# Kernel tuning notes

Hardware: AMD Instinct MI355X
Metric: run time of the kernel (lower is better)

Reference implementation:

```python
import jax, jax.numpy as jnp
import numpy as np

N_TOKENS = 16384
HIDDEN = 1024
FFN = 4096
N_EXPERTS = 8
TOP_K = 2


def setup_inputs() -> dict:
    key = jax.random.key(0)
    k_x, k_r, k_w1, k_w2 = jax.random.split(key, 4)
    x = jax.random.normal(k_x, (N_TOKENS, HIDDEN), dtype=jnp.float32)
    w_router = jax.random.normal(k_r, (HIDDEN, N_EXPERTS), dtype=jnp.float32) * (HIDDEN ** -0.5)
    w1 = jax.random.normal(k_w1, (N_EXPERTS, HIDDEN, FFN), dtype=jnp.float32) * (HIDDEN ** -0.5)
    w2 = jax.random.normal(k_w2, (N_EXPERTS, FFN, HIDDEN), dtype=jnp.float32) * (FFN ** -0.5)
    return {"x": x, "w_router": w_router, "w1": w1, "w2": w2}


def reference(x, w_router, w1, w2):
    # --- TopKRouter: softmax over experts, take top-k, renormalize ---
    logits = x @ w_router                              # [N, E]
    probs = jax.nn.softmax(logits, axis=-1)
    topk_w, topk_idx = jax.lax.top_k(probs, TOP_K)     # [N, K]
    topk_w = topk_w / jnp.sum(topk_w, axis=-1, keepdims=True)

    # --- dispatch -> per-expert FFN -> weighted combine ---
    # Single-device equivalent: the all-to-all + sort/unsort (pt_dispatch/
    # pt_combine) form an identity permutation pair, so the math reduces to:
    # out[n] = sum_k topk_w[n,k] * FFN_{topk_idx[n,k]}(x[n])
    out = jnp.zeros_like(x)
    n_experts = w1.shape[0]
    for e in range(n_experts):  # small fixed expert loop (grouped GEMM)
        # combine weight this expert contributes to each token
        coeff = jnp.sum(jnp.where(topk_idx == e, topk_w, 0.0), axis=-1)  # [N]
        y = jax.nn.gelu(x @ w1[e]) @ w2[e]                               # [N, H]
        out = out + coeff[:, None] * y
    return out
```

## Files before the change

kernel.cpp:

```cpp
#include <hip/hip_runtime.h>
#include <cstdint>
#include <cstddef>

#define N_TOKENS 16384
#define HIDDEN 1024
#define FFN 4096
#define NEXP 8
#define BM 128
#define BK 32
#define MAXR (N_TOKENS*2 + NEXP*BM)
#define MAXTILES (MAXR/BM)

typedef __bf16 bf16;
typedef __attribute__((ext_vector_type(8))) __bf16 bf16x8;
typedef __attribute__((ext_vector_type(4))) __bf16 bf16x4;
typedef __attribute__((ext_vector_type(4))) float f32x4;

__device__ __forceinline__ void gload16(const void* g, void* l) {
  __builtin_amdgcn_global_load_lds((const __attribute__((address_space(1))) void*)g,
                                   (__attribute__((address_space(3))) void*)l, 16, 0, 0);
}

__device__ __forceinline__ int xcd_swz(int orig, int nwg) {
  int q = nwg >> 3, r = nwg & 7;
  int xcd = orig & 7, idx = orig >> 3;
  int base = (xcd < r) ? xcd * (q + 1) : r * (q + 1) + (xcd - r) * q;
  return base + idx;
}


__global__ __launch_bounds__(256) void convx_k(const float* __restrict__ x,
                                               bf16* __restrict__ xb) {
  int i = blockIdx.x * 256 + threadIdx.x;
  float4 v = reinterpret_cast<const float4*>(x)[i];
  bf16x4 o = { (bf16)v.x, (bf16)v.y, (bf16)v.z, (bf16)v.w };
  *reinterpret_cast<bf16x4*>(xb + (size_t)i * 4) = o;
}

__global__ __launch_bounds__(256) void transconv_k(const float* __restrict__ src,
                                                   bf16* __restrict__ dst,
                                                   int R, int C) {
  __shared__ float tile[64][65];
  int bx = blockIdx.x * 64;
  int by = blockIdx.y * 64;
  const float* s = src + (size_t)blockIdx.z * R * C;
  bf16* d = dst + (size_t)blockIdx.z * R * C;
  int tid = threadIdx.x;
  int tc = (tid & 15) * 4;
  int tr = tid >> 4;
  #pragma unroll
  for (int p = 0; p < 4; ++p) {
    int r = p * 16 + tr;
    float4 v = *reinterpret_cast<const float4*>(s + (size_t)(by + r) * C + bx + tc);
    tile[r][tc] = v.x; tile[r][tc + 1] = v.y; tile[r][tc + 2] = v.z; tile[r][tc + 3] = v.w;
  }
  __syncthreads();
  int wr = (tid & 15) * 4;
  int wc = tid >> 4;
  #pragma unroll
  for (int p = 0; p < 4; ++p) {
    int c = p * 16 + wc;
    bf16x4 o = { (bf16)tile[wr][c], (bf16)tile[wr + 1][c],
                 (bf16)tile[wr + 2][c], (bf16)tile[wr + 3][c] };
    *reinterpret_cast<bf16x4*>(d + (size_t)(bx + c) * R + by + wr) = o;
  }
}


__global__ __launch_bounds__(256) void logits_k(const float* __restrict__ x,
                                                const float* __restrict__ wrt,
                                                double* __restrict__ logitsE) {
  __shared__ float wT[NEXP][HIDDEN + 1];
  int tid = threadIdx.x;
  for (int i = tid; i < HIDDEN * NEXP; i += 256) {
    int k = i >> 3, e = i & 7;
    wT[e][k] = wrt[i];
  }
  __syncthreads();
  int t = blockIdx.x * 32 + (tid >> 3);
  int e = tid & 7;
  int goff = ((tid >> 3) & 7) * 4;
  const float* xr = x + (size_t)t * HIDDEN;
  double acc = 0.0;
  #pragma unroll 4
  for (int k = 0; k < HIDDEN; k += 4) {
    int kk = (k + goff) & (HIDDEN - 1);
    float4 v = *reinterpret_cast<const float4*>(xr + kk);
    acc += (double)v.x * (double)wT[e][kk];
    acc += (double)v.y * (double)wT[e][kk + 1];
    acc += (double)v.z * (double)wT[e][kk + 2];
    acc += (double)v.w * (double)wT[e][kk + 3];
  }
  logitsE[(size_t)e * N_TOKENS + t] = acc;
}


__global__ __launch_bounds__(256) void route_k(const double* __restrict__ logitsE,
                                               int* __restrict__ expIdx,
                                               float* __restrict__ expW,
                                               int* __restrict__ counts) {
  __shared__ int lcnt[NEXP];
  int tid = threadIdx.x;
  if (tid < NEXP) lcnt[tid] = 0;
  __syncthreads();
  int n = blockIdx.x * 256 + tid;
  double lg[NEXP];
  #pragma unroll
  for (int e = 0; e < NEXP; ++e) lg[e] = logitsE[(size_t)e * N_TOKENS + n];
  int e1 = 0;
  #pragma unroll
  for (int e = 1; e < NEXP; ++e) if (lg[e] > lg[e1]) e1 = e;
  int e2 = (e1 == 0) ? 1 : 0;
  #pragma unroll
  for (int e = 0; e < NEXP; ++e)
    if (e != e1 && e != e2 && lg[e] > lg[e2]) e2 = e;
  double d = lg[e2] - lg[e1];
  float w1v = (float)(1.0 / (1.0 + exp(d)));
  expIdx[2 * n]     = e1; expIdx[2 * n + 1] = e2;
  expW[2 * n]       = w1v; expW[2 * n + 1]  = 1.0f - w1v;
  atomicAdd(&lcnt[e1], 1);
  atomicAdd(&lcnt[e2], 1);
  __syncthreads();
  if (tid < NEXP) atomicAdd(&counts[tid], lcnt[tid]);
}


__global__ void offsets_k(const int* __restrict__ counts,
                          int* __restrict__ padOff, int* __restrict__ cursor) {
  if (threadIdx.x == 0) {
    int o = 0;
    for (int e = 0; e < NEXP; ++e) {
      padOff[e] = o;
      o += ((counts[e] + BM - 1) / BM) * BM;
    }
    padOff[NEXP] = o;
  }
  if (threadIdx.x < NEXP) cursor[threadIdx.x] = 0;
}

__global__ __launch_bounds__(256) void scatter_k(const int* __restrict__ expIdx,
                                                 const float* __restrict__ expW,
                                                 const int* __restrict__ padOff,
                                                 int* __restrict__ cursor,
                                                 int* __restrict__ rowTok,
                                                 float* __restrict__ rowW,
                                                 int* __restrict__ tokRow) {
  __shared__ int lcnt[NEXP], lbase[NEXP];
  int tid = threadIdx.x;
  if (tid < NEXP) lcnt[tid] = 0;
  __syncthreads();
  int n = blockIdx.x * 256 + tid;
  int e0 = expIdx[2 * n], e1 = expIdx[2 * n + 1];
  float w0 = expW[2 * n], w1 = expW[2 * n + 1];
  int p0 = atomicAdd(&lcnt[e0], 1);
  int p1 = atomicAdd(&lcnt[e1], 1);
  __syncthreads();
  if (tid < NEXP) lbase[tid] = atomicAdd(&cursor[tid], lcnt[tid]);
  __syncthreads();
  int r0 = padOff[e0] + lbase[e0] + p0;
  int r1 = padOff[e1] + lbase[e1] + p1;
  rowTok[r0] = n;  rowW[r0] = w0;  tokRow[2 * n]     = r0;
  rowTok[r1] = n;  rowW[r1] = w1;  tokRow[2 * n + 1] = r1;
}


__device__ __forceinline__ float gelu_tanh(float v) {
  float c = 0.7978845608028654f * (v + 0.044715f * v * v * v);
  c = fminf(fmaxf(c, -15.f), 15.f);
  float ex = __expf(2.f * c);
  float t = (ex - 1.f) / (ex + 1.f);
  return 0.5f * v * (1.f + t);
}

__global__ __launch_bounds__(256, 2) void gemm1_k(const bf16* __restrict__ xb,
                                                  const bf16* __restrict__ w1bT,
                                                  bf16* __restrict__ h,
                                                  const int* __restrict__ rowTok,
                                                  const int* __restrict__ padOff,
                                                  int tileStart, int rowStart) {
  __shared__ __attribute__((aligned(16))) bf16 As[BM * BK];
  __shared__ __attribute__((aligned(16))) bf16 Bs[BM * BK];
  const int nCT = FFN / 128;
  int wg = xcd_swz((int)blockIdx.x, (int)gridDim.x);
  int bt = tileStart + wg / nCT;
  int ct = wg % nCT;
  int r0 = bt * BM;
  if (r0 >= padOff[NEXP]) return;
  int e = 0;
  while (padOff[e + 1] <= r0) ++e;

  int tid = threadIdx.x;
  int lane = tid & 63, wave = tid >> 6;
  const bf16* Bbase = w1bT + ((size_t)e * FFN + (size_t)ct * 128) * HIDDEN;

  const bf16* aSrc[2]; const bf16* bSrc[2]; int ldsOff[2];
  #pragma unroll
  for (int j = 0; j < 2; ++j) {
    int ci = wave * 128 + j * 64 + lane;
    int r = ci >> 2, s = ci & 3;
    int ks = s ^ ((r >> 1) & 3);
    int tok = rowTok[r0 + r]; if (tok < 0) tok = 0;
    aSrc[j] = xb + (size_t)tok * HIDDEN + ks * 8;
    bSrc[j] = Bbase + (size_t)r * HIDDEN + ks * 8;
    ldsOff[j] = (wave * 128 + j * 64) * 8;
  }
  int g = lane >> 4, lr = lane & 15;
  int wr = wave >> 1, wc = wave & 1;
  int aOff[4], bOff[4];
  #pragma unroll
  for (int m = 0; m < 4; ++m) { int r = wr * 64 + m * 16 + lr; aOff[m] = r * BK + ((g ^ ((r >> 1) & 3)) << 3); }
  #pragma unroll
  for (int n = 0; n < 4; ++n) { int r = wc * 64 + n * 16 + lr; bOff[n] = r * BK + ((g ^ ((r >> 1) & 3)) << 3); }

  f32x4 zero = {0.f, 0.f, 0.f, 0.f};
  f32x4 acc[4][4];
  #pragma unroll
  for (int m = 0; m < 4; ++m)
    #pragma unroll
    for (int n = 0; n < 4; ++n) acc[m][n] = zero;

  for (int k0 = 0; k0 < HIDDEN; k0 += BK) {
    #pragma unroll
    for (int j = 0; j < 2; ++j) {
      gload16(aSrc[j] + k0, &As[ldsOff[j]]);
      gload16(bSrc[j] + k0, &Bs[ldsOff[j]]);
    }
    __syncthreads();
    bf16x8 af[4], bfr[4];
    #pragma unroll
    for (int m = 0; m < 4; ++m) af[m] = *reinterpret_cast<const bf16x8*>(&As[aOff[m]]);
    #pragma unroll
    for (int n = 0; n < 4; ++n) bfr[n] = *reinterpret_cast<const bf16x8*>(&Bs[bOff[n]]);
    #pragma unroll
    for (int m = 0; m < 4; ++m)
      #pragma unroll
      for (int n = 0; n < 4; ++n)
        acc[m][n] = __builtin_amdgcn_mfma_f32_16x16x32_bf16(af[m], bfr[n], acc[m][n], 0, 0, 0);
    __syncthreads();
  }

  int colBase = ct * 128 + wc * 64 + lr;
  #pragma unroll
  for (int m = 0; m < 4; ++m) {
    #pragma unroll
    for (int i = 0; i < 4; ++i) {
      int t = r0 + wr * 64 + m * 16 + g * 4 + i;
      bf16* hp = h + (size_t)(t - rowStart) * FFN + colBase;
      #pragma unroll
      for (int n = 0; n < 4; ++n)
        hp[n * 16] = (bf16)gelu_tanh(acc[m][n][i]);
    }
  }
}


__global__ __launch_bounds__(256, 2) void gemm2_k(const bf16* __restrict__ h,
                                                  const bf16* __restrict__ w2bT,
                                                  float* __restrict__ y,
                                                  const int* __restrict__ padOff,
                                                  int tileStart, int rowStart) {
  __shared__ __attribute__((aligned(16))) bf16 As[BM * BK];
  __shared__ __attribute__((aligned(16))) bf16 Bs[BM * BK];
  const int nCT = HIDDEN / 128;
  int wg = xcd_swz((int)blockIdx.x, (int)gridDim.x);
  int bt = tileStart + wg / nCT;
  int ct = wg % nCT;
  int r0 = bt * BM;
  if (r0 >= padOff[NEXP]) return;
  int e = 0;
  while (padOff[e + 1] <= r0) ++e;

  int tid = threadIdx.x;
  int lane = tid & 63, wave = tid >> 6;
  const bf16* Bbase = w2bT + ((size_t)e * HIDDEN + (size_t)ct * 128) * FFN;
  const bf16* Arow = h + (size_t)(r0 - rowStart) * FFN;

  const bf16* aSrc[2]; const bf16* bSrc[2]; int ldsOff[2];
  #pragma unroll
  for (int j = 0; j < 2; ++j) {
    int ci = wave * 128 + j * 64 + lane;
    int r = ci >> 2, s = ci & 3;
    int ks = s ^ ((r >> 1) & 3);
    aSrc[j] = Arow + (size_t)r * FFN + ks * 8;
    bSrc[j] = Bbase + (size_t)r * FFN + ks * 8;
    ldsOff[j] = (wave * 128 + j * 64) * 8;
  }
  int g = lane >> 4, lr = lane & 15;
  int wr = wave >> 1, wc = wave & 1;
  int aOff[4], bOff[4];
  #pragma unroll
  for (int m = 0; m < 4; ++m) { int r = wr * 64 + m * 16 + lr; aOff[m] = r * BK + ((g ^ ((r >> 1) & 3)) << 3); }
  #pragma unroll
  for (int n = 0; n < 4; ++n) { int r = wc * 64 + n * 16 + lr; bOff[n] = r * BK + ((g ^ ((r >> 1) & 3)) << 3); }

  f32x4 zero = {0.f, 0.f, 0.f, 0.f};
  f32x4 acc[4][4];
  #pragma unroll
  for (int m = 0; m < 4; ++m)
    #pragma unroll
    for (int n = 0; n < 4; ++n) acc[m][n] = zero;

  for (int k0 = 0; k0 < FFN; k0 += BK) {
    #pragma unroll
    for (int j = 0; j < 2; ++j) {
      gload16(aSrc[j] + k0, &As[ldsOff[j]]);
      gload16(bSrc[j] + k0, &Bs[ldsOff[j]]);
    }
    __syncthreads();
    bf16x8 af[4], bfr[4];
    #pragma unroll
    for (int m = 0; m < 4; ++m) af[m] = *reinterpret_cast<const bf16x8*>(&As[aOff[m]]);
    #pragma unroll
    for (int n = 0; n < 4; ++n) bfr[n] = *reinterpret_cast<const bf16x8*>(&Bs[bOff[n]]);
    #pragma unroll
    for (int m = 0; m < 4; ++m)
      #pragma unroll
      for (int n = 0; n < 4; ++n)
        acc[m][n] = __builtin_amdgcn_mfma_f32_16x16x32_bf16(af[m], bfr[n], acc[m][n], 0, 0, 0);
    __syncthreads();
  }

  int colBase = ct * 128 + wc * 64 + lr;
  #pragma unroll
  for (int m = 0; m < 4; ++m) {
    #pragma unroll
    for (int i = 0; i < 4; ++i) {
      int t = r0 + wr * 64 + m * 16 + g * 4 + i;
      float* yp = y + (size_t)t * HIDDEN + colBase;
      #pragma unroll
      for (int n = 0; n < 4; ++n)
        yp[n * 16] = acc[m][n][i];
    }
  }
}


__global__ __launch_bounds__(256) void combine_k(const float* __restrict__ y,
                                                 const int* __restrict__ tokRow,
                                                 const float* __restrict__ rowW,
                                                 float* __restrict__ out) {
  int n = blockIdx.x;
  int c = threadIdx.x * 4;
  int r0 = tokRow[2 * n], r1 = tokRow[2 * n + 1];
  float w0 = rowW[r0], w1 = rowW[r1];
  float4 a = *reinterpret_cast<const float4*>(y + (size_t)r0 * HIDDEN + c);
  float4 b = *reinterpret_cast<const float4*>(y + (size_t)r1 * HIDDEN + c);
  float4 o = { w0 * a.x + w1 * b.x, w0 * a.y + w1 * b.y,
               w0 * a.z + w1 * b.z, w0 * a.w + w1 * b.w };
  *reinterpret_cast<float4*>(out + (size_t)n * HIDDEN + c) = o;
}


extern "C" void kernel_launch(void* const* d_in, const int* in_sizes, int n_in,
                              void* d_out, int out_size, void* d_ws, size_t ws_size,
                              hipStream_t stream) {
  const float* x   = (const float*)d_in[0];
  const float* wrt = (const float*)d_in[1];
  const float* w1  = (const float*)d_in[2];
  const float* w2  = (const float*)d_in[3];
  float* out = (float*)d_out;

  char* p = (char*)d_ws;
  size_t off = 0;
  auto alloc = [&](size_t bytes) -> void* {
    void* r = p + off;
    off = (off + bytes + 255) & ~(size_t)255;
    return r;
  };

  int*    counts  = (int*)   alloc(NEXP * 4);
  int*    padOff  = (int*)   alloc((NEXP + 1) * 4);
  int*    cursor  = (int*)   alloc(NEXP * 4);
  int*    expIdx  = (int*)   alloc((size_t)N_TOKENS * 2 * 4);
  float*  expW    = (float*) alloc((size_t)N_TOKENS * 2 * 4);
  int*    rowTok  = (int*)   alloc((size_t)MAXR * 4);
  float*  rowW    = (float*) alloc((size_t)MAXR * 4);
  int*    tokRow  = (int*)   alloc((size_t)N_TOKENS * 2 * 4);
  double* logitsE = (double*)alloc((size_t)NEXP * N_TOKENS * 8);
  bf16*   xb      = (bf16*)  alloc((size_t)N_TOKENS * HIDDEN * 2);
  bf16*   w1bT    = (bf16*)  alloc((size_t)NEXP * FFN * HIDDEN * 2);
  bf16*   w2bT    = (bf16*)  alloc((size_t)NEXP * FFN * HIDDEN * 2);
  float*  y       = (float*) alloc((size_t)MAXR * HIDDEN * 4);
  size_t fixed = off;
  bf16* h = (bf16*)(p + fixed);

  size_t tileB = (size_t)BM * FFN * 2;
  size_t avail = (ws_size > fixed) ? (ws_size - fixed) : tileB;
  size_t fitSz = avail / tileB;
  int tilesFit = (int)((fitSz < (size_t)MAXTILES) ? fitSz : (size_t)MAXTILES);
  if (tilesFit < 1) tilesFit = 1;
  int nchunks = (MAXTILES + tilesFit - 1) / tilesFit;
  int tpc = (MAXTILES + nchunks - 1) / nchunks;

  hipMemsetAsync(counts, 0, NEXP * 4, stream);
  hipMemsetAsync(rowTok, 0xFF, (size_t)MAXR * 4, stream);

  convx_k<<<N_TOKENS * HIDDEN / 4 / 256, 256, 0, stream>>>(x, xb);
  transconv_k<<<dim3(FFN / 64, HIDDEN / 64, NEXP), dim3(256, 1, 1), 0, stream>>>(w1, w1bT, HIDDEN, FFN);
  transconv_k<<<dim3(HIDDEN / 64, FFN / 64, NEXP), dim3(256, 1, 1), 0, stream>>>(w2, w2bT, FFN, HIDDEN);
  logits_k<<<N_TOKENS / 32, 256, 0, stream>>>(x, wrt, logitsE);
  route_k<<<N_TOKENS / 256, 256, 0, stream>>>(logitsE, expIdx, expW, counts);
  offsets_k<<<1, 64, 0, stream>>>(counts, padOff, cursor);
  scatter_k<<<N_TOKENS / 256, 256, 0, stream>>>(expIdx, expW, padOff, cursor, rowTok, rowW, tokRow);

  for (int c = 0; c < nchunks; ++c) {
    int ts = c * tpc;
    int rs = ts * BM;
    gemm1_k<<<tpc * (FFN / 128), 256, 0, stream>>>(xb, w1bT, h, rowTok, padOff, ts, rs);
    gemm2_k<<<tpc * (HIDDEN / 128), 256, 0, stream>>>(h, w2bT, y, padOff, ts, rs);
  }
  combine_k<<<N_TOKENS, 256, 0, stream>>>(y, tokRow, rowW, out);
}
```

Measured before the change: 1.015 ms.

## Use 256x256 tiles with a 4-stage async LDS pipeline and bf16 expert outputs

```diff
diff --git a/kernel.cpp b/kernel.cpp
--- a/kernel.cpp
+++ b/kernel.cpp
@@ -6,10 +6,10 @@
 #define HIDDEN 1024
 #define FFN 4096
 #define NEXP 8
-#define BM 128
+#define BM2 256
 #define BK 32
-#define MAXR (N_TOKENS*2 + NEXP*BM)
-#define MAXTILES (MAXR/BM)
+#define MAXR (N_TOKENS*2 + NEXP*BM2)
+#define MAXTILES (MAXR/BM2)
 
 typedef __bf16 bf16;
 typedef __attribute__((ext_vector_type(8))) __bf16 bf16x8;
@@ -131,7 +131,7 @@
     int o = 0;
     for (int e = 0; e < NEXP; ++e) {
       padOff[e] = o;
-      o += ((counts[e] + BM - 1) / BM) * BM;
+      o += ((counts[e] + BM2 - 1) / BM2) * BM2;
     }
     padOff[NEXP] = o;
   }
@@ -164,6 +164,74 @@
 }
 
 
+#define GEMM_PROLOGUE(AROWPTR_EXPR, BROW_STRIDE)                               \
+  int tid = threadIdx.x;                                                       \
+  int lane = tid & 63, wave = tid >> 6;                                        \
+  int wm = wave >> 2, wn = wave & 3;                                           \
+  int lr = lane & 15, g = lane >> 4;                                           \
+  const bf16* aPtr[2]; const bf16* bPtr[2];                                    \
+  int aLds[2], bLds[2];                                                        \
+  _Pragma("unroll")                                                            \
+  for (int j = 0; j < 2; ++j) {                                                \
+    int ci = j * 512 + tid;                                                    \
+    int r = ci >> 2, s = ci & 3;                                               \
+    int ks = s ^ (r & 3);                                                      \
+    aPtr[j] = (AROWPTR_EXPR) + ks * 8;                                         \
+    bPtr[j] = Bbase + (size_t)r * (BROW_STRIDE) + ks * 8;                      \
+    aLds[j] = j * 4096 + wave * 512;                                           \
+    bLds[j] = j * 4096 + wave * 512;                                           \
+  }                                                                            \
+  int aRd = (wm * 128 + lr) * BK + ((g ^ (lr & 3)) << 3);                      \
+  int bRd = (wn * 64 + lr) * BK + ((g ^ (lr & 3)) << 3);                       \
+  f32x4 acc[8][4];                                                             \
+  _Pragma("unroll")                                                            \
+  for (int m = 0; m < 8; ++m)                                                  \
+    _Pragma("unroll")                                                          \
+    for (int n = 0; n < 4; ++n) acc[m][n] = (f32x4){0.f, 0.f, 0.f, 0.f};
+
+#define STAGE(kt, b) do {                                                      \
+    gload16(aPtr[0] + (size_t)(kt) * BK, &Ab[b][aLds[0]]);                     \
+    gload16(aPtr[1] + (size_t)(kt) * BK, &Ab[b][aLds[1]]);                     \
+    gload16(bPtr[0] + (size_t)(kt) * BK, &Bb[b][bLds[0]]);                     \
+    gload16(bPtr[1] + (size_t)(kt) * BK, &Bb[b][bLds[1]]);                     \
+  } while (0)
+
+#define GEMM_KLOOP(NT)                                                         \
+  STAGE(0, 0); STAGE(1, 1); STAGE(2, 2);                                       \
+  _Pragma("unroll 1")                                                          \
+  for (int kt = 0; kt < (NT); ++kt) {                                          \
+    int b = kt & 3;                                                            \
+    int pf = kt + 3;                                                           \
+    if (pf < (NT)) STAGE(pf, pf & 3);                                          \
+    int rem = (NT) - 1 - kt;                                                   \
+    if (rem >= 3)      asm volatile("s_waitcnt vmcnt(12)" ::: "memory");       \
+    else if (rem == 2) asm volatile("s_waitcnt vmcnt(8)" ::: "memory");        \
+    else if (rem == 1) asm volatile("s_waitcnt vmcnt(4)" ::: "memory");        \
+    else               asm volatile("s_waitcnt vmcnt(0)" ::: "memory");        \
+    __builtin_amdgcn_sched_barrier(0);                                         \
+    __builtin_amdgcn_s_barrier();                                              \
+    __builtin_amdgcn_sched_barrier(0);                                         \
+    bf16x8 af[8], bf[4];                                                       \
+    _Pragma("unroll")                                                          \
+    for (int m = 0; m < 8; ++m)                                                \
+      af[m] = *reinterpret_cast<const bf16x8*>(&Ab[b][aRd + m * 512]);         \
+    _Pragma("unroll")                                                          \
+    for (int n = 0; n < 4; ++n)                                                \
+      bf[n] = *reinterpret_cast<const bf16x8*>(&Bb[b][bRd + n * 512]);         \
+    __builtin_amdgcn_s_setprio(1);                                             \
+    _Pragma("unroll")                                                          \
+    for (int m = 0; m < 8; ++m)                                                \
+      _Pragma("unroll")                                                        \
+      for (int n = 0; n < 4; ++n)                                              \
+        acc[m][n] = __builtin_amdgcn_mfma_f32_16x16x32_bf16(af[m], bf[n],      \
+                                                            acc[m][n], 0, 0, 0); \
+    __builtin_amdgcn_s_setprio(0);                                             \
+    __builtin_amdgcn_sched_barrier(0);                                         \
+    __builtin_amdgcn_s_barrier();                                              \
+    __builtin_amdgcn_sched_barrier(0);                                         \
+  }
+
+
 __device__ __forceinline__ float gelu_tanh(float v) {
   float c = 0.7978845608028654f * (v + 0.044715f * v * v * v);
   c = fminf(fmaxf(c, -15.f), 15.f);
@@ -172,79 +240,34 @@
   return 0.5f * v * (1.f + t);
 }
 
-__global__ __launch_bounds__(256, 2) void gemm1_k(const bf16* __restrict__ xb,
+__global__ __launch_bounds__(512, 2) void gemm1_k(const bf16* __restrict__ xb,
                                                   const bf16* __restrict__ w1bT,
                                                   bf16* __restrict__ h,
                                                   const int* __restrict__ rowTok,
                                                   const int* __restrict__ padOff,
                                                   int tileStart, int rowStart) {
-  __shared__ __attribute__((aligned(16))) bf16 As[BM * BK];
-  __shared__ __attribute__((aligned(16))) bf16 Bs[BM * BK];
-  const int nCT = FFN / 128;
+  __shared__ __attribute__((aligned(16))) bf16 Ab[4][256 * BK];
+  __shared__ __attribute__((aligned(16))) bf16 Bb[4][256 * BK];
+  const int nCT = FFN / 256;
   int wg = xcd_swz((int)blockIdx.x, (int)gridDim.x);
   int bt = tileStart + wg / nCT;
   int ct = wg % nCT;
-  int r0 = bt * BM;
+  int r0 = bt * BM2;
   if (r0 >= padOff[NEXP]) return;
   int e = 0;
   while (padOff[e + 1] <= r0) ++e;
-
-  int tid = threadIdx.x;
-  int lane = tid & 63, wave = tid >> 6;
-  const bf16* Bbase = w1bT + ((size_t)e * FFN + (size_t)ct * 128) * HIDDEN;
-
-  const bf16* aSrc[2]; const bf16* bSrc[2]; int ldsOff[2];
-  #pragma unroll
-  for (int j = 0; j < 2; ++j) {
-    int ci = wave * 128 + j * 64 + lane;
-    int r = ci >> 2, s = ci & 3;
-    int ks = s ^ ((r >> 1) & 3);
-    int tok = rowTok[r0 + r]; if (tok < 0) tok = 0;
-    aSrc[j] = xb + (size_t)tok * HIDDEN + ks * 8;
-    bSrc[j] = Bbase + (size_t)r * HIDDEN + ks * 8;
-    ldsOff[j] = (wave * 128 + j * 64) * 8;
-  }
-  int g = lane >> 4, lr = lane & 15;
-  int wr = wave >> 1, wc = wave & 1;
-  int aOff[4], bOff[4];
-  #pragma unroll
-  for (int m = 0; m < 4; ++m) { int r = wr * 64 + m * 16 + lr; aOff[m] = r * BK + ((g ^ ((r >> 1) & 3)) << 3); }
-  #pragma unroll
-  for (int n = 0; n < 4; ++n) { int r = wc * 64 + n * 16 + lr; bOff[n] = r * BK + ((g ^ ((r >> 1) & 3)) << 3); }
-
-  f32x4 zero = {0.f, 0.f, 0.f, 0.f};
-  f32x4 acc[4][4];
-  #pragma unroll
-  for (int m = 0; m < 4; ++m)
-    #pragma unroll
-    for (int n = 0; n < 4; ++n) acc[m][n] = zero;
-
-  for (int k0 = 0; k0 < HIDDEN; k0 += BK) {
-    #pragma unroll
-    for (int j = 0; j < 2; ++j) {
-      gload16(aSrc[j] + k0, &As[ldsOff[j]]);
-      gload16(bSrc[j] + k0, &Bs[ldsOff[j]]);
-    }
-    __syncthreads();
-    bf16x8 af[4], bfr[4];
-    #pragma unroll
-    for (int m = 0; m < 4; ++m) af[m] = *reinterpret_cast<const bf16x8*>(&As[aOff[m]]);
-    #pragma unroll
-    for (int n = 0; n < 4; ++n) bfr[n] = *reinterpret_cast<const bf16x8*>(&Bs[bOff[n]]);
-    #pragma unroll
-    for (int m = 0; m < 4; ++m)
-      #pragma unroll
-      for (int n = 0; n < 4; ++n)
-        acc[m][n] = __builtin_amdgcn_mfma_f32_16x16x32_bf16(af[m], bfr[n], acc[m][n], 0, 0, 0);
-    __syncthreads();
-  }
-
-  int colBase = ct * 128 + wc * 64 + lr;
-  #pragma unroll
-  for (int m = 0; m < 4; ++m) {
+  const bf16* Bbase = w1bT + ((size_t)e * FFN + (size_t)ct * 256) * HIDDEN;
+
+  GEMM_PROLOGUE(xb + (size_t)(rowTok[r0 + r] < 0 ? 0 : rowTok[r0 + r]) * HIDDEN,
+                HIDDEN)
+  GEMM_KLOOP(HIDDEN / BK)
+
+  int colBase = ct * 256 + wn * 64 + lr;
+  #pragma unroll
+  for (int m = 0; m < 8; ++m) {
     #pragma unroll
     for (int i = 0; i < 4; ++i) {
-      int t = r0 + wr * 64 + m * 16 + g * 4 + i;
+      int t = r0 + wm * 128 + m * 16 + g * 4 + i;
       bf16* hp = h + (size_t)(t - rowStart) * FFN + colBase;
       #pragma unroll
       for (int n = 0; n < 4; ++n)
@@ -254,88 +277,42 @@
 }
 
 
-__global__ __launch_bounds__(256, 2) void gemm2_k(const bf16* __restrict__ h,
+__global__ __launch_bounds__(512, 2) void gemm2_k(const bf16* __restrict__ h,
                                                   const bf16* __restrict__ w2bT,
-                                                  float* __restrict__ y,
+                                                  bf16* __restrict__ y,
                                                   const int* __restrict__ padOff,
                                                   int tileStart, int rowStart) {
-  __shared__ __attribute__((aligned(16))) bf16 As[BM * BK];
-  __shared__ __attribute__((aligned(16))) bf16 Bs[BM * BK];
-  const int nCT = HIDDEN / 128;
+  __shared__ __attribute__((aligned(16))) bf16 Ab[4][256 * BK];
+  __shared__ __attribute__((aligned(16))) bf16 Bb[4][256 * BK];
+  const int nCT = HIDDEN / 256;
   int wg = xcd_swz((int)blockIdx.x, (int)gridDim.x);
   int bt = tileStart + wg / nCT;
   int ct = wg % nCT;
-  int r0 = bt * BM;
+  int r0 = bt * BM2;
   if (r0 >= padOff[NEXP]) return;
   int e = 0;
   while (padOff[e + 1] <= r0) ++e;
-
-  int tid = threadIdx.x;
-  int lane = tid & 63, wave = tid >> 6;
-  const bf16* Bbase = w2bT + ((size_t)e * HIDDEN + (size_t)ct * 128) * FFN;
-  const bf16* Arow = h + (size_t)(r0 - rowStart) * FFN;
-
-  const bf16* aSrc[2]; const bf16* bSrc[2]; int ldsOff[2];
-  #pragma unroll
-  for (int j = 0; j < 2; ++j) {
-    int ci = wave * 128 + j * 64 + lane;
-    int r = ci >> 2, s = ci & 3;
-    int ks = s ^ ((r >> 1) & 3);
-    aSrc[j] = Arow + (size_t)r * FFN + ks * 8;
-    bSrc[j] = Bbase + (size_t)r * FFN + ks * 8;
-    ldsOff[j] = (wave * 128 + j * 64) * 8;
-  }
-  int g = lane >> 4, lr = lane & 15;
-  int wr = wave >> 1, wc = wave & 1;
-  int aOff[4], bOff[4];
-  #pragma unroll
-  for (int m = 0; m < 4; ++m) { int r = wr * 64 + m * 16 + lr; aOff[m] = r * BK + ((g ^ ((r >> 1) & 3)) << 3); }
-  #pragma unroll
-  for (int n = 0; n < 4; ++n) { int r = wc * 64 + n * 16 + lr; bOff[n] = r * BK + ((g ^ ((r >> 1) & 3)) << 3); }
-
-  f32x4 zero = {0.f, 0.f, 0.f, 0.f};
-  f32x4 acc[4][4];
-  #pragma unroll
-  for (int m = 0; m < 4; ++m)
+  const bf16* Bbase = w2bT + ((size_t)e * HIDDEN + (size_t)ct * 256) * FFN;
+
+  GEMM_PROLOGUE(h + (size_t)(r0 - rowStart + r) * FFN, FFN)
+  GEMM_KLOOP(FFN / BK)
+
+  int colBase = ct * 256 + wn * 64 + lr;
+  #pragma unroll
+  for (int m = 0; m < 8; ++m) {
     #pragma unroll
-    for (int n = 0; n < 4; ++n) acc[m][n] = zero;
-
-  for (int k0 = 0; k0 < FFN; k0 += BK) {
-    #pragma unroll
-    for (int j = 0; j < 2; ++j) {
-      gload16(aSrc[j] + k0, &As[ldsOff[j]]);
-      gload16(bSrc[j] + k0, &Bs[ldsOff[j]]);
-    }
-    __syncthreads();
-    bf16x8 af[4], bfr[4];
-    #pragma unroll
-    for (int m = 0; m < 4; ++m) af[m] = *reinterpret_cast<const bf16x8*>(&As[aOff[m]]);
-    #pragma unroll
-    for (int n = 0; n < 4; ++n) bfr[n] = *reinterpret_cast<const bf16x8*>(&Bs[bOff[n]]);
-    #pragma unroll
-    for (int m = 0; m < 4; ++m)
+    for (int i = 0; i < 4; ++i) {
+      int t = r0 + wm * 128 + m * 16 + g * 4 + i;
+      bf16* yp = y + (size_t)t * HIDDEN + colBase;
       #pragma unroll
       for (int n = 0; n < 4; ++n)
-        acc[m][n] = __builtin_amdgcn_mfma_f32_16x16x32_bf16(af[m], bfr[n], acc[m][n], 0, 0, 0);
-    __syncthreads();
-  }
-
-  int colBase = ct * 128 + wc * 64 + lr;
-  #pragma unroll
-  for (int m = 0; m < 4; ++m) {
-    #pragma unroll
-    for (int i = 0; i < 4; ++i) {
-      int t = r0 + wr * 64 + m * 16 + g * 4 + i;
-      float* yp = y + (size_t)t * HIDDEN + colBase;
-      #pragma unroll
-      for (int n = 0; n < 4; ++n)
-        yp[n * 16] = acc[m][n][i];
+        yp[n * 16] = (bf16)acc[m][n][i];
     }
   }
 }
 
 
-__global__ __launch_bounds__(256) void combine_k(const float* __restrict__ y,
+__global__ __launch_bounds__(256) void combine_k(const bf16* __restrict__ y,
                                                  const int* __restrict__ tokRow,
                                                  const float* __restrict__ rowW,
                                                  float* __restrict__ out) {
@@ -343,10 +320,10 @@
   int c = threadIdx.x * 4;
   int r0 = tokRow[2 * n], r1 = tokRow[2 * n + 1];
   float w0 = rowW[r0], w1 = rowW[r1];
-  float4 a = *reinterpret_cast<const float4*>(y + (size_t)r0 * HIDDEN + c);
-  float4 b = *reinterpret_cast<const float4*>(y + (size_t)r1 * HIDDEN + c);
-  float4 o = { w0 * a.x + w1 * b.x, w0 * a.y + w1 * b.y,
-               w0 * a.z + w1 * b.z, w0 * a.w + w1 * b.w };
+  bf16x4 a = *reinterpret_cast<const bf16x4*>(y + (size_t)r0 * HIDDEN + c);
+  bf16x4 b = *reinterpret_cast<const bf16x4*>(y + (size_t)r1 * HIDDEN + c);
+  float4 o = { w0 * (float)a[0] + w1 * (float)b[0], w0 * (float)a[1] + w1 * (float)b[1],
+               w0 * (float)a[2] + w1 * (float)b[2], w0 * (float)a[3] + w1 * (float)b[3] };
   *reinterpret_cast<float4*>(out + (size_t)n * HIDDEN + c) = o;
 }
 
@@ -380,11 +357,11 @@
   bf16*   xb      = (bf16*)  alloc((size_t)N_TOKENS * HIDDEN * 2);
   bf16*   w1bT    = (bf16*)  alloc((size_t)NEXP * FFN * HIDDEN * 2);
   bf16*   w2bT    = (bf16*)  alloc((size_t)NEXP * FFN * HIDDEN * 2);
-  float*  y       = (float*) alloc((size_t)MAXR * HIDDEN * 4);
+  bf16*   y       = (bf16*)  alloc((size_t)MAXR * HIDDEN * 2);
   size_t fixed = off;
   bf16* h = (bf16*)(p + fixed);
 
-  size_t tileB = (size_t)BM * FFN * 2;
+  size_t tileB = (size_t)BM2 * FFN * 2;
   size_t avail = (ws_size > fixed) ? (ws_size - fixed) : tileB;
   size_t fitSz = avail / tileB;
   int tilesFit = (int)((fitSz < (size_t)MAXTILES) ? fitSz : (size_t)MAXTILES);
@@ -405,9 +382,9 @@
 
   for (int c = 0; c < nchunks; ++c) {
     int ts = c * tpc;
-    int rs = ts * BM;
-    gemm1_k<<<tpc * (FFN / 128), 256, 0, stream>>>(xb, w1bT, h, rowTok, padOff, ts, rs);
-    gemm2_k<<<tpc * (HIDDEN / 128), 256, 0, stream>>>(h, w2bT, y, padOff, ts, rs);
+    int rs = ts * BM2;
+    gemm1_k<<<tpc * (FFN / 256), 512, 0, stream>>>(xb, w1bT, h, rowTok, padOff, ts, rs);
+    gemm2_k<<<tpc * (HIDDEN / 256), 512, 0, stream>>>(h, w2bT, y, padOff, ts, rs);
   }
   combine_k<<<N_TOKENS, 256, 0, stream>>>(y, tokRow, rowW, out);
 }
```

Measured after the change: 1.206 ms. +18.8%, slower.

## Triple-buffer LDS loads in expert GEMMs and store expert outputs as bf16

Applied to the files above, without the earlier changes.

```diff
diff --git a/kernel.cpp b/kernel.cpp
--- a/kernel.cpp
+++ b/kernel.cpp
@@ -7,7 +7,7 @@
 #define FFN 4096
 #define NEXP 8
 #define BM 128
-#define BK 32
+#define BKS 32
 #define MAXR (N_TOKENS*2 + NEXP*BM)
 #define MAXTILES (MAXR/BM)
 
@@ -172,14 +172,14 @@
   return 0.5f * v * (1.f + t);
 }
 
-__global__ __launch_bounds__(256, 2) void gemm1_k(const bf16* __restrict__ xb,
+__global__ __launch_bounds__(256, 3) void gemm1_k(const bf16* __restrict__ xb,
                                                   const bf16* __restrict__ w1bT,
                                                   bf16* __restrict__ h,
                                                   const int* __restrict__ rowTok,
                                                   const int* __restrict__ padOff,
                                                   int tileStart, int rowStart) {
-  __shared__ __attribute__((aligned(16))) bf16 As[BM * BK];
-  __shared__ __attribute__((aligned(16))) bf16 Bs[BM * BK];
+  __shared__ __attribute__((aligned(16))) bf16 Ab[3][BM * BKS];
+  __shared__ __attribute__((aligned(16))) bf16 Bb[3][BM * BKS];
   const int nCT = FFN / 128;
   int wg = xcd_swz((int)blockIdx.x, (int)gridDim.x);
   int bt = tileStart + wg / nCT;
@@ -188,63 +188,78 @@
   if (r0 >= padOff[NEXP]) return;
   int e = 0;
   while (padOff[e + 1] <= r0) ++e;
+  const bf16* Bbase = w1bT + ((size_t)e * FFN + (size_t)ct * 128) * HIDDEN;
 
   int tid = threadIdx.x;
   int lane = tid & 63, wave = tid >> 6;
-  const bf16* Bbase = w1bT + ((size_t)e * FFN + (size_t)ct * 128) * HIDDEN;
-
-  const bf16* aSrc[2]; const bf16* bSrc[2]; int ldsOff[2];
+  const bf16* aPtr[2]; const bf16* bPtr[2]; int ldsOff[2];
   #pragma unroll
   for (int j = 0; j < 2; ++j) {
-    int ci = wave * 128 + j * 64 + lane;
-    int r = ci >> 2, s = ci & 3;
-    int ks = s ^ ((r >> 1) & 3);
+    int ci = j * 256 + tid;
+    int r = ci >> 2, sg = ci & 3;
+    int ks = sg ^ ((r >> 1) & 3);
     int tok = rowTok[r0 + r]; if (tok < 0) tok = 0;
-    aSrc[j] = xb + (size_t)tok * HIDDEN + ks * 8;
-    bSrc[j] = Bbase + (size_t)r * HIDDEN + ks * 8;
-    ldsOff[j] = (wave * 128 + j * 64) * 8;
-  }
-  int g = lane >> 4, lr = lane & 15;
-  int wr = wave >> 1, wc = wave & 1;
+    aPtr[j] = xb + (size_t)tok * HIDDEN + ks * 8;
+    bPtr[j] = Bbase + (size_t)r * HIDDEN + ks * 8;
+    ldsOff[j] = ci * 8;
+  }
+  int lr = lane & 15, g = lane >> 4;
+  int wm = wave >> 1, wn = wave & 1;
   int aOff[4], bOff[4];
   #pragma unroll
-  for (int m = 0; m < 4; ++m) { int r = wr * 64 + m * 16 + lr; aOff[m] = r * BK + ((g ^ ((r >> 1) & 3)) << 3); }
-  #pragma unroll
-  for (int n = 0; n < 4; ++n) { int r = wc * 64 + n * 16 + lr; bOff[n] = r * BK + ((g ^ ((r >> 1) & 3)) << 3); }
-
-  f32x4 zero = {0.f, 0.f, 0.f, 0.f};
+  for (int m = 0; m < 4; ++m) { int r = wm * 64 + m * 16 + lr; aOff[m] = r * BKS + ((g ^ ((r >> 1) & 3)) << 3); }
+  #pragma unroll
+  for (int n = 0; n < 4; ++n) { int r = wn * 64 + n * 16 + lr; bOff[n] = r * BKS + ((g ^ ((r >> 1) & 3)) << 3); }
+
   f32x4 acc[4][4];
   #pragma unroll
   for (int m = 0; m < 4; ++m)
     #pragma unroll
-    for (int n = 0; n < 4; ++n) acc[m][n] = zero;
-
-  for (int k0 = 0; k0 < HIDDEN; k0 += BK) {
-    #pragma unroll
-    for (int j = 0; j < 2; ++j) {
-      gload16(aSrc[j] + k0, &As[ldsOff[j]]);
-      gload16(bSrc[j] + k0, &Bs[ldsOff[j]]);
-    }
-    __syncthreads();
+    for (int n = 0; n < 4; ++n) acc[m][n] = (f32x4){0.f, 0.f, 0.f, 0.f};
+
+  const int NT = HIDDEN / BKS;
+  auto stage = [&](int sl, int b) {
+    #pragma unroll
+    for (int j = 0; j < 2; ++j) gload16(aPtr[j] + (size_t)sl * BKS, &Ab[b][ldsOff[j]]);
+    #pragma unroll
+    for (int j = 0; j < 2; ++j) gload16(bPtr[j] + (size_t)sl * BKS, &Bb[b][ldsOff[j]]);
+  };
+  stage(0, 0); stage(1, 1);
+  int buf = 0, sbuf = 2;
+  #pragma unroll 1
+  for (int s = 0; s < NT; ++s) {
+    if (s + 2 < NT) stage(s + 2, sbuf);
+    if (s < NT - 2)       asm volatile("s_waitcnt vmcnt(8)" ::: "memory");
+    else if (s == NT - 2) asm volatile("s_waitcnt vmcnt(4)" ::: "memory");
+    else                  asm volatile("s_waitcnt vmcnt(0)" ::: "memory");
+    __builtin_amdgcn_sched_barrier(0);
+    __builtin_amdgcn_s_barrier();
+    __builtin_amdgcn_sched_barrier(0);
     bf16x8 af[4], bfr[4];
     #pragma unroll
-    for (int m = 0; m < 4; ++m) af[m] = *reinterpret_cast<const bf16x8*>(&As[aOff[m]]);
-    #pragma unroll
-    for (int n = 0; n < 4; ++n) bfr[n] = *reinterpret_cast<const bf16x8*>(&Bs[bOff[n]]);
+    for (int m = 0; m < 4; ++m) af[m] = *reinterpret_cast<const bf16x8*>(&Ab[buf][aOff[m]]);
+    #pragma unroll
+    for (int n = 0; n < 4; ++n) bfr[n] = *reinterpret_cast<const bf16x8*>(&Bb[buf][bOff[n]]);
+    __builtin_amdgcn_s_setprio(1);
     #pragma unroll
     for (int m = 0; m < 4; ++m)
       #pragma unroll
       for (int n = 0; n < 4; ++n)
         acc[m][n] = __builtin_amdgcn_mfma_f32_16x16x32_bf16(af[m], bfr[n], acc[m][n], 0, 0, 0);
-    __syncthreads();
-  }
-
-  int colBase = ct * 128 + wc * 64 + lr;
+    __builtin_amdgcn_s_setprio(0);
+    __builtin_amdgcn_sched_barrier(0);
+    __builtin_amdgcn_s_barrier();
+    __builtin_amdgcn_sched_barrier(0);
+    buf = (buf == 2) ? 0 : buf + 1;
+    sbuf = (sbuf == 2) ? 0 : sbuf + 1;
+  }
+
+  int colBase = ct * 128 + wn * 64 + lr;
   #pragma unroll
   for (int m = 0; m < 4; ++m) {
     #pragma unroll
     for (int i = 0; i < 4; ++i) {
-      int t = r0 + wr * 64 + m * 16 + g * 4 + i;
+      int t = r0 + wm * 64 + m * 16 + g * 4 + i;
       bf16* hp = h + (size_t)(t - rowStart) * FFN + colBase;
       #pragma unroll
       for (int n = 0; n < 4; ++n)
@@ -253,14 +268,13 @@
   }
 }
 
-
-__global__ __launch_bounds__(256, 2) void gemm2_k(const bf16* __restrict__ h,
+__global__ __launch_bounds__(256, 3) void gemm2_k(const bf16* __restrict__ h,
                                                   const bf16* __restrict__ w2bT,
-                                                  float* __restrict__ y,
+                                                  bf16* __restrict__ y,
                                                   const int* __restrict__ padOff,
                                                   int tileStart, int rowStart) {
-  __shared__ __attribute__((aligned(16))) bf16 As[BM * BK];
-  __shared__ __attribute__((aligned(16))) bf16 Bs[BM * BK];
+  __shared__ __attribute__((aligned(16))) bf16 Ab[3][BM * BKS];
+  __shared__ __attribute__((aligned(16))) bf16 Bb[3][BM * BKS];
   const int nCT = HIDDEN / 128;
   int wg = xcd_swz((int)blockIdx.x, (int)gridDim.x);
   int bt = tileStart + wg / nCT;
@@ -269,73 +283,88 @@
   if (r0 >= padOff[NEXP]) return;
   int e = 0;
   while (padOff[e + 1] <= r0) ++e;
-
-  int tid = threadIdx.x;
-  int lane = tid & 63, wave = tid >> 6;
   const bf16* Bbase = w2bT + ((size_t)e * HIDDEN + (size_t)ct * 128) * FFN;
   const bf16* Arow = h + (size_t)(r0 - rowStart) * FFN;
 
-  const bf16* aSrc[2]; const bf16* bSrc[2]; int ldsOff[2];
+  int tid = threadIdx.x;
+  int lane = tid & 63, wave = tid >> 6;
+  const bf16* aPtr[2]; const bf16* bPtr[2]; int ldsOff[2];
   #pragma unroll
   for (int j = 0; j < 2; ++j) {
-    int ci = wave * 128 + j * 64 + lane;
-    int r = ci >> 2, s = ci & 3;
-    int ks = s ^ ((r >> 1) & 3);
-    aSrc[j] = Arow + (size_t)r * FFN + ks * 8;
-    bSrc[j] = Bbase + (size_t)r * FFN + ks * 8;
-    ldsOff[j] = (wave * 128 + j * 64) * 8;
-  }
-  int g = lane >> 4, lr = lane & 15;
-  int wr = wave >> 1, wc = wave & 1;
+    int ci = j * 256 + tid;
+    int r = ci >> 2, sg = ci & 3;
+    int ks = sg ^ ((r >> 1) & 3);
+    aPtr[j] = Arow + (size_t)r * FFN + ks * 8;
+    bPtr[j] = Bbase + (size_t)r * FFN + ks * 8;
+    ldsOff[j] = ci * 8;
+  }
+  int lr = lane & 15, g = lane >> 4;
+  int wm = wave >> 1, wn = wave & 1;
   int aOff[4], bOff[4];
   #pragma unroll
-  for (int m = 0; m < 4; ++m) { int r = wr * 64 + m * 16 + lr; aOff[m] = r * BK + ((g ^ ((r >> 1) & 3)) << 3); }
-  #pragma unroll
-  for (int n = 0; n < 4; ++n) { int r = wc * 64 + n * 16 + lr; bOff[n] = r * BK + ((g ^ ((r >> 1) & 3)) << 3); }
-
-  f32x4 zero = {0.f, 0.f, 0.f, 0.f};
+  for (int m = 0; m < 4; ++m) { int r = wm * 64 + m * 16 + lr; aOff[m] = r * BKS + ((g ^ ((r >> 1) & 3)) << 3); }
+  #pragma unroll
+  for (int n = 0; n < 4; ++n) { int r = wn * 64 + n * 16 + lr; bOff[n] = r * BKS + ((g ^ ((r >> 1) & 3)) << 3); }
+
   f32x4 acc[4][4];
   #pragma unroll
   for (int m = 0; m < 4; ++m)
     #pragma unroll
-    for (int n = 0; n < 4; ++n) acc[m][n] = zero;
-
-  for (int k0 = 0; k0 < FFN; k0 += BK) {
-    #pragma unroll
-    for (int j = 0; j < 2; ++j) {
-      gload16(aSrc[j] + k0, &As[ldsOff[j]]);
-      gload16(bSrc[j] + k0, &Bs[ldsOff[j]]);
-    }
-    __syncthreads();
+    for (int n = 0; n < 4; ++n) acc[m][n] = (f32x4){0.f, 0.f, 0.f, 0.f};
+
+  const int NT = FFN / BKS;
+  auto stage = [&](int sl, int b) {
+    #pragma unroll
+    for (int j = 0; j < 2; ++j) gload16(aPtr[j] + (size_t)sl * BKS, &Ab[b][ldsOff[j]]);
+    #pragma unroll
+    for (int j = 0; j < 2; ++j) gload16(bPtr[j] + (size_t)sl * BKS, &Bb[b][ldsOff[j]]);
+  };
+  stage(0, 0); stage(1, 1);
+  int buf = 0, sbuf = 2;
+  #pragma unroll 1
+  for (int s = 0; s < NT; ++s) {
+    if (s + 2 < NT) stage(s + 2, sbuf);
+    if (s < NT - 2)       asm volatile("s_waitcnt vmcnt(8)" ::: "memory");
+    else if (s == NT - 2) asm volatile("s_waitcnt vmcnt(4)" ::: "memory");
+    else                  asm volatile("s_waitcnt vmcnt(0)" ::: "memory");
+    __builtin_amdgcn_sched_barrier(0);
+    __builtin_amdgcn_s_barrier();
+    __builtin_amdgcn_sched_barrier(0);
     bf16x8 af[4], bfr[4];
     #pragma unroll
-    for (int m = 0; m < 4; ++m) af[m] = *reinterpret_cast<const bf16x8*>(&As[aOff[m]]);
-    #pragma unroll
-    for (int n = 0; n < 4; ++n) bfr[n] = *reinterpret_cast<const bf16x8*>(&Bs[bOff[n]]);
+    for (int m = 0; m < 4; ++m) af[m] = *reinterpret_cast<const bf16x8*>(&Ab[buf][aOff[m]]);
+    #pragma unroll
+    for (int n = 0; n < 4; ++n) bfr[n] = *reinterpret_cast<const bf16x8*>(&Bb[buf][bOff[n]]);
+    __builtin_amdgcn_s_setprio(1);
     #pragma unroll
     for (int m = 0; m < 4; ++m)
       #pragma unroll
       for (int n = 0; n < 4; ++n)
         acc[m][n] = __builtin_amdgcn_mfma_f32_16x16x32_bf16(af[m], bfr[n], acc[m][n], 0, 0, 0);
-    __syncthreads();
-  }
-
-  int colBase = ct * 128 + wc * 64 + lr;
+    __builtin_amdgcn_s_setprio(0);
+    __builtin_amdgcn_sched_barrier(0);
+    __builtin_amdgcn_s_barrier();
+    __builtin_amdgcn_sched_barrier(0);
+    buf = (buf == 2) ? 0 : buf + 1;
+    sbuf = (sbuf == 2) ? 0 : sbuf + 1;
+  }
+
+  int colBase = ct * 128 + wn * 64 + lr;
   #pragma unroll
   for (int m = 0; m < 4; ++m) {
     #pragma unroll
     for (int i = 0; i < 4; ++i) {
-      int t = r0 + wr * 64 + m * 16 + g * 4 + i;
-      float* yp = y + (size_t)t * HIDDEN + colBase;
+      int t = r0 + wm * 64 + m * 16 + g * 4 + i;
+      bf16* yp = y + (size_t)t * HIDDEN + colBase;
       #pragma unroll
       for (int n = 0; n < 4; ++n)
-        yp[n * 16] = acc[m][n][i];
+        yp[n * 16] = (bf16)acc[m][n][i];
     }
   }
 }
 
 
-__global__ __launch_bounds__(256) void combine_k(const float* __restrict__ y,
+__global__ __launch_bounds__(256) void combine_k(const bf16* __restrict__ y,
                                                  const int* __restrict__ tokRow,
                                                  const float* __restrict__ rowW,
                                                  float* __restrict__ out) {
@@ -343,10 +372,10 @@
   int c = threadIdx.x * 4;
   int r0 = tokRow[2 * n], r1 = tokRow[2 * n + 1];
   float w0 = rowW[r0], w1 = rowW[r1];
-  float4 a = *reinterpret_cast<const float4*>(y + (size_t)r0 * HIDDEN + c);
-  float4 b = *reinterpret_cast<const float4*>(y + (size_t)r1 * HIDDEN + c);
-  float4 o = { w0 * a.x + w1 * b.x, w0 * a.y + w1 * b.y,
-               w0 * a.z + w1 * b.z, w0 * a.w + w1 * b.w };
+  bf16x4 a = *reinterpret_cast<const bf16x4*>(y + (size_t)r0 * HIDDEN + c);
+  bf16x4 b = *reinterpret_cast<const bf16x4*>(y + (size_t)r1 * HIDDEN + c);
+  float4 o = { w0 * (float)a[0] + w1 * (float)b[0], w0 * (float)a[1] + w1 * (float)b[1],
+               w0 * (float)a[2] + w1 * (float)b[2], w0 * (float)a[3] + w1 * (float)b[3] };
   *reinterpret_cast<float4*>(out + (size_t)n * HIDDEN + c) = o;
 }
 
@@ -380,7 +409,7 @@
   bf16*   xb      = (bf16*)  alloc((size_t)N_TOKENS * HIDDEN * 2);
   bf16*   w1bT    = (bf16*)  alloc((size_t)NEXP * FFN * HIDDEN * 2);
   bf16*   w2bT    = (bf16*)  alloc((size_t)NEXP * FFN * HIDDEN * 2);
-  float*  y       = (float*) alloc((size_t)MAXR * HIDDEN * 4);
+  bf16*   y       = (bf16*)  alloc((size_t)MAXR * HIDDEN * 2);
   size_t fixed = off;
   bf16* h = (bf16*)(p + fixed);
 
```

Result: faster. 943.1 us (-7.1%).
